# Kernel optimization log

Hardware: AMD Instinct MI355X
Metric: run time of the kernel (lower is better)

## Reference

```python
import jax, jax.numpy as jnp
import numpy as np

EPS = 1e-10


def _entropy(feat):
    # feat: [B,S,D] -> [B,S]
    fa = jnp.abs(feat)
    fn = fa / (fa.sum(axis=-1, keepdims=True) + EPS)
    return -jnp.sum(fn * jnp.log(fn + EPS), axis=-1)


def setup_inputs() -> dict:
    key = jax.random.key(0)
    ks = jax.random.split(key, 16)
    B, S, H, C = 16, 1024, 512, 7
    inp = {
        'text': jax.random.normal(ks[0], (B, S, H), dtype=jnp.float32),
        'audio': jax.random.normal(ks[1], (B, S, H), dtype=jnp.float32),
        'visual': jax.random.normal(ks[2], (B, S, H), dtype=jnp.float32),
        'speaker_graph': jax.random.uniform(ks[3], (B, S, S), dtype=jnp.float32),
        'temporal_graph': jax.random.uniform(ks[4], (B, S, S), dtype=jnp.float32),
        'qmask': jax.random.randint(ks[5], (B, S), 0, 9, dtype=jnp.int64),
        # entropy gate linear: in = 3H+1, out = H  (stored as [in,out])
        'gate_W': jax.random.normal(ks[6], (3 * H + 1, H), dtype=jnp.float32) * 0.02,
        'gate_b': jnp.zeros((H,), dtype=jnp.float32),
        # spectral conv layers
        'W0': jax.random.normal(ks[7], (3 * H, H), dtype=jnp.float32) * 0.02,
        'b0': jnp.zeros((H,), dtype=jnp.float32),
        'W1': jax.random.normal(ks[8], (H, H), dtype=jnp.float32) * 0.02,
        'b1': jnp.zeros((H,), dtype=jnp.float32),
        'W2': jax.random.normal(ks[9], (H, H), dtype=jnp.float32) * 0.02,
        'b2': jnp.zeros((H,), dtype=jnp.float32),
        # classifier
        'Wc': jax.random.normal(ks[10], (H, C), dtype=jnp.float32) * 0.02,
        'bc': jnp.zeros((C,), dtype=jnp.float32),
    }
    return inp


def reference(text, audio, visual, speaker_graph, temporal_graph, qmask,
              gate_W, gate_b, W0, b0, W1, b1, W2, b2, Wc, bc):
    feats = {'text': text, 'audio': audio, 'visual': visual}
    names = list(feats.keys())

    # per-node entropy on speaker graph path (entropy_t computed but unused, as in source)
    ent_s = {m: _entropy(f) for m, f in feats.items()}

    # entropy-weighted gating per modality
    fused = {}
    for m in names:
        feat = feats[m]
        ref = jnp.mean(jnp.stack([feats[o] for o in names if o != m], axis=-1), axis=-1)
        gi = jnp.concatenate([feat, feat, ref, ent_s[m][..., None]], axis=-1)  # [B,S,3H+1]
        gate = jax.nn.sigmoid(gi @ gate_W + gate_b)
        fused[m] = gate * feat

    # spectral GNN: symmetric-normalized fused adjacency with self loops
    B, S = text.shape[0], text.shape[1]
    fused_adj = 0.5 * speaker_graph + 0.5 * temporal_graph
    fused_adj = fused_adj + jnp.eye(S, dtype=fused_adj.dtype)[None]
    D = fused_adj.sum(axis=-1)                                   # [B,S]
    dsi = jax.lax.rsqrt(D + EPS)                                  # (D+eps)^-0.5
    norm_adj = dsi[:, :, None] * fused_adj * dsi[:, None, :]      # [B,S,S]

    h = jnp.concatenate([fused['text'], fused['audio'], fused['visual']], axis=-1)  # [B,S,3H]
    for W, b in ((W0, b0), (W1, b1), (W2, b2)):
        h = jax.nn.relu(jnp.einsum('bij,bjd->bid', norm_adj, h @ W) + b)

    return h @ Wc + bc
```

## Files before the change

kernel.cpp:

```cpp
#include <hip/hip_runtime.h>
#include <hip/hip_bf16.h>
#include <hip/hip_fp16.h>

typedef _Float16 f16;
typedef __attribute__((ext_vector_type(8))) _Float16 f16x8;
typedef __attribute__((ext_vector_type(4))) _Float16 f16x4;
typedef __attribute__((ext_vector_type(4))) float f32x4;
typedef __attribute__((address_space(1))) const unsigned int gu32;
typedef __attribute__((address_space(3))) unsigned int lu32;

#define BQ 16
#define SQ 1024
#define HQ 512
#define MQ (BQ*SQ)
#define PLANE ((size_t)MQ*512)

#define OFF_WG1T 0ul
#define OFF_WG2T 524288ul
#define OFF_W0T  1048576ul
#define OFF_W1T  2621440ul
#define OFF_W2T  3145728ul
#define OFF_WENT 3670016ul
#define OFF_ENTS 3672064ul
#define OFF_DSI  3868672ul
#define OFF_XF16 3934208ul
#define OFF_ANORM OFF_XF16
#define OFF_HN   (OFF_XF16 + 33554432ul)
#define OFF_T    71043072ul
#define OFF_YT   OFF_T
#define OFF_HCAT 104597504ul

__device__ __forceinline__ void gl16(f16* lds, const f16* g) {
    __builtin_amdgcn_global_load_lds(
        (gu32*)(const __attribute__((address_space(1))) f16*)g,
        (lu32*)(__attribute__((address_space(3))) f16*)lds, 16, 0, 0);
}

__global__ __launch_bounds__(256) void k_prep(
    const float* __restrict__ gW, const float* __restrict__ W0,
    const float* __restrict__ W1, const float* __restrict__ W2,
    f16* __restrict__ Wg1t, f16* __restrict__ Wg2t, f16* __restrict__ W0t,
    f16* __restrict__ W1t, f16* __restrict__ W2t, float* __restrict__ went)
{
    int i = blockIdx.x * 256 + threadIdx.x;
    if (i < 1536*512) {
        int n = i & 511, k = i >> 9;
        W0t[(size_t)n*1536 + k] = (f16)W0[(size_t)k*512 + n];
    }
    if (i < 512*512) {
        int n = i >> 9, k = i & 511;
        float wa = gW[(size_t)k*512 + n];
        float wb = gW[(size_t)(512 + k)*512 + n];
        float wr = gW[(size_t)(1024 + k)*512 + n];
        Wg1t[(size_t)n*512 + k] = (f16)(wa + wb - 0.5f*wr);
        Wg2t[(size_t)n*512 + k] = (f16)(0.5f*wr);
        W1t[(size_t)n*512 + k]  = (f16)W1[(size_t)k*512 + n];
        W2t[(size_t)n*512 + k]  = (f16)W2[(size_t)k*512 + n];
    }
    if (i < 512) went[i] = gW[(size_t)1536*512 + i];
}

__global__ __launch_bounds__(256) void k_ent(
    const float* __restrict__ t, const float* __restrict__ a, const float* __restrict__ v,
    f16* __restrict__ xf, float* __restrict__ ents)
{
    int wave = threadIdx.x >> 6, lane = threadIdx.x & 63;
    int row = blockIdx.x * 4 + wave;
    const float* ptrs[3] = {t, a, v};
    float sum8[8];
#pragma unroll
    for (int j = 0; j < 8; j++) sum8[j] = 0.f;
#pragma unroll
    for (int m = 0; m < 3; m++) {
        const float4* p = (const float4*)(ptrs[m] + (size_t)row*512);
        float4 x0 = p[lane*2], x1 = p[lane*2 + 1];
        float xs[8] = {x0.x,x0.y,x0.z,x0.w,x1.x,x1.y,x1.z,x1.w};
        float s = 0.f;
#pragma unroll
        for (int j = 0; j < 8; j++) s += fabsf(xs[j]);
#pragma unroll
        for (int off = 32; off; off >>= 1) s += __shfl_xor(s, off);
        float inv = 1.f / (s + 1e-10f);
        float e = 0.f;
#pragma unroll
        for (int j = 0; j < 8; j++) { float fn = fabsf(xs[j])*inv; e += fn*__logf(fn + 1e-10f); }
#pragma unroll
        for (int off = 32; off; off >>= 1) e += __shfl_xor(e, off);
        if (lane == 0) ents[m*MQ + row] = -e;
        f16x8 o;
#pragma unroll
        for (int j = 0; j < 8; j++) o[j] = (f16)xs[j];
        *(f16x8*)(xf + ((size_t)m*MQ + row)*512 + lane*8) = o;
#pragma unroll
        for (int j = 0; j < 8; j++) sum8[j] += xs[j];
    }
    f16x8 o;
#pragma unroll
    for (int j = 0; j < 8; j++) o[j] = (f16)sum8[j];
    *(f16x8*)(xf + ((size_t)3*MQ + row)*512 + lane*8) = o;
}

__global__ __launch_bounds__(256) void k_dsi(
    const float* __restrict__ sp, const float* __restrict__ tg, float* __restrict__ dsi)
{
    int wave = threadIdx.x >> 6, lane = threadIdx.x & 63;
    int row = blockIdx.x * 4 + wave;
    const float4* p1 = (const float4*)(sp + (size_t)row*1024);
    const float4* p2 = (const float4*)(tg + (size_t)row*1024);
    float s = 0.f;
#pragma unroll
    for (int c = 0; c < 4; c++) {
        float4 x = p1[c*64 + lane], y = p2[c*64 + lane];
        s += x.x + x.y + x.z + x.w + y.x + y.y + y.z + y.w;
    }
#pragma unroll
    for (int off = 32; off; off >>= 1) s += __shfl_xor(s, off);
    if (lane == 0) dsi[row] = 1.f / sqrtf(0.5f*s + 1.f + 1e-10f);
}

__global__ __launch_bounds__(256) void k_anorm(
    const float* __restrict__ sp, const float* __restrict__ tg,
    const float* __restrict__ dsi, f16* __restrict__ an)
{
    size_t t = (size_t)blockIdx.x*256 + threadIdx.x;
    int j4 = (int)(t & 255) * 4;
    int i  = (int)(t >> 8) & 1023;
    int b  = (int)(t >> 18);
    size_t base = ((size_t)b << 20) + (size_t)i*1024 + j4;
    float4 x = *(const float4*)(sp + base);
    float4 y = *(const float4*)(tg + base);
    float4 dj = *(const float4*)(dsi + b*1024 + j4);
    float di = dsi[b*1024 + i];
    float v0 = 0.5f*(x.x + y.x) + (i == j4+0 ? 1.f : 0.f);
    float v1 = 0.5f*(x.y + y.y) + (i == j4+1 ? 1.f : 0.f);
    float v2 = 0.5f*(x.z + y.z) + (i == j4+2 ? 1.f : 0.f);
    float v3 = 0.5f*(x.w + y.w) + (i == j4+3 ? 1.f : 0.f);
    f16x4 o;
    o[0] = (f16)(di*v0*dj.x); o[1] = (f16)(di*v1*dj.y);
    o[2] = (f16)(di*v2*dj.z); o[3] = (f16)(di*v3*dj.w);
    *(f16x4*)(an + base) = o;
}

template<int MODE>
__global__ __launch_bounds__(256) void k_gemm(
    const f16* __restrict__ A, const f16* __restrict__ Bt, int K,
    const f16* __restrict__ Tbuf, const float* __restrict__ entS,
    const float* __restrict__ went, const float* __restrict__ gb,
    const f16* __restrict__ featf, f16* __restrict__ hOut, int hColOff,
    const float* __restrict__ bias)
{
    __shared__ f16 As[128*64];
    __shared__ f16 Bs[128*64];
    int tid = threadIdx.x;
    int lane = tid & 63, wave = tid >> 6;
    int wr = wave >> 1, wc = wave & 1;
    int m0 = blockIdx.x * 128, n0 = blockIdx.y * 128;
    int z = blockIdx.z;
    if constexpr (MODE == 3) {
        A  += (size_t)z * (1024*1024);
        Bt += (size_t)z * (512*1024);
    }
    int lrow = lane >> 3;
    int swz  = (lane & 7) ^ lrow;
    const f16* pA = A  + (size_t)(m0 + wave*32 + lrow)*K + swz*8;
    const f16* pB = Bt + (size_t)(n0 + wave*32 + lrow)*K + swz*8;
    f16* lA = As + (wave*4)*512;
    f16* lB = Bs + (wave*4)*512;

    f32x4 acc[4][4];
#pragma unroll
    for (int mi = 0; mi < 4; mi++)
#pragma unroll
        for (int ni = 0; ni < 4; ni++) acc[mi][ni] = (f32x4){0.f,0.f,0.f,0.f};
    int g = lane >> 4, r = lane & 15;

    for (int kt = 0; kt < K; kt += 64) {
        __syncthreads();
#pragma unroll
        for (int j = 0; j < 4; j++) {
            gl16(lA + j*512, pA + (size_t)(j*8)*K + kt);
            gl16(lB + j*512, pB + (size_t)(j*8)*K + kt);
        }
        __syncthreads();
#pragma unroll
        for (int kk = 0; kk < 2; kk++) {
            f16x8 af[4], bf[4];
#pragma unroll
            for (int mi = 0; mi < 4; mi++) {
                int row = wr*64 + mi*16 + r;
                int ch = (kk*4 + g) ^ (row & 7);
                af[mi] = *(const f16x8*)&As[row*64 + ch*8];
            }
#pragma unroll
            for (int ni = 0; ni < 4; ni++) {
                int row = wc*64 + ni*16 + r;
                int ch = (kk*4 + g) ^ (row & 7);
                bf[ni] = *(const f16x8*)&Bs[row*64 + ch*8];
            }
#pragma unroll
            for (int mi = 0; mi < 4; mi++)
#pragma unroll
                for (int ni = 0; ni < 4; ni++)
                    acc[mi][ni] = __builtin_amdgcn_mfma_f32_16x16x32_f16(af[mi], bf[ni], acc[mi][ni], 0, 0, 0);
        }
    }
#pragma unroll
    for (int mi = 0; mi < 4; mi++) {
        int row0 = m0 + wr*64 + mi*16 + g*4;
#pragma unroll
        for (int ni = 0; ni < 4; ni++) {
            int col = n0 + wc*64 + ni*16 + r;
            f32x4 v = acc[mi][ni];
            if constexpr (MODE == 0) {
#pragma unroll
                for (int j = 0; j < 4; j++)
                    hOut[(size_t)(row0 + j)*512 + col] = (f16)v[j];
            } else if constexpr (MODE == 1) {
                float wcol = went[col], gbc = gb[col];
#pragma unroll
                for (int j = 0; j < 4; j++) {
                    int row = row0 + j;
                    float val = v[j] + (float)Tbuf[(size_t)row*512 + col] + entS[row]*wcol + gbc;
                    float gate = 1.f / (1.f + __expf(-val));
                    float o = gate * (float)featf[(size_t)row*512 + col];
                    hOut[(size_t)row*1536 + hColOff + col] = (f16)o;
                }
            } else if constexpr (MODE == 2) {
                int bb = row0 >> 10, ml = row0 & 1023;
                f16x4 h4;
#pragma unroll
                for (int j = 0; j < 4; j++) h4[j] = (f16)v[j];
                *(f16x4*)(hOut + (((size_t)(bb*512 + col)) << 10) + ml) = h4;
            } else {
                float bcol = bias[col];
#pragma unroll
                for (int j = 0; j < 4; j++) {
                    float o = v[j] + bcol;
                    o = o > 0.f ? o : 0.f;
                    hOut[(size_t)(z*1024 + row0 + j)*512 + col] = (f16)o;
                }
            }
        }
    }
}

__global__ __launch_bounds__(256) void k_cls(
    const f16* __restrict__ h, const float* __restrict__ Wc,
    const float* __restrict__ bc, float* __restrict__ out)
{
    int wave = threadIdx.x >> 6, lane = threadIdx.x & 63;
    int row = blockIdx.x * 4 + wave;
    f16x8 hv = *(const f16x8*)(h + (size_t)row*512 + lane*8);
    float acc[7];
#pragma unroll
    for (int c = 0; c < 7; c++) acc[c] = 0.f;
#pragma unroll
    for (int j = 0; j < 8; j++) {
        float x = (float)hv[j];
        const float* wrow = Wc + (size_t)(lane*8 + j)*7;
#pragma unroll
        for (int c = 0; c < 7; c++) acc[c] += x * wrow[c];
    }
#pragma unroll
    for (int off = 32; off; off >>= 1)
#pragma unroll
        for (int c = 0; c < 7; c++) acc[c] += __shfl_xor(acc[c], off);
    if (lane == 0) {
#pragma unroll
        for (int c = 0; c < 7; c++) out[(size_t)row*7 + c] = acc[c] + bc[c];
    }
}

extern "C" void kernel_launch(void* const* d_in, const int* in_sizes, int n_in,
                              void* d_out, int out_size, void* d_ws, size_t ws_size,
                              hipStream_t stream) {
    (void)in_sizes; (void)n_in; (void)out_size; (void)ws_size;
    const float* text   = (const float*)d_in[0];
    const float* audio  = (const float*)d_in[1];
    const float* visual = (const float*)d_in[2];
    const float* spg    = (const float*)d_in[3];
    const float* tmg    = (const float*)d_in[4];
    const float* gW     = (const float*)d_in[6];
    const float* gb     = (const float*)d_in[7];
    const float* W0     = (const float*)d_in[8];
    const float* b0     = (const float*)d_in[9];
    const float* W1     = (const float*)d_in[10];
    const float* b1     = (const float*)d_in[11];
    const float* W2     = (const float*)d_in[12];
    const float* b2     = (const float*)d_in[13];
    const float* Wc     = (const float*)d_in[14];
    const float* bc     = (const float*)d_in[15];

    char* ws = (char*)d_ws;
    f16*   Wg1t = (f16*)(ws + OFF_WG1T);
    f16*   Wg2t = (f16*)(ws + OFF_WG2T);
    f16*   W0t  = (f16*)(ws + OFF_W0T);
    f16*   W1t  = (f16*)(ws + OFF_W1T);
    f16*   W2t  = (f16*)(ws + OFF_W2T);
    float* went = (float*)(ws + OFF_WENT);
    float* ents = (float*)(ws + OFF_ENTS);
    float* dsi  = (float*)(ws + OFF_DSI);
    f16*   xf   = (f16*)(ws + OFF_XF16);
    f16*   an   = (f16*)(ws + OFF_ANORM);
    f16*   hn   = (f16*)(ws + OFF_HN);
    f16*   Tbuf = (f16*)(ws + OFF_T);
    f16*   yt   = (f16*)(ws + OFF_YT);
    f16*   hcat = (f16*)(ws + OFF_HCAT);
    float* outp = (float*)d_out;

    dim3 blk(256);
    k_prep<<<3072, blk, 0, stream>>>(gW, W0, W1, W2, Wg1t, Wg2t, W0t, W1t, W2t, went);
    k_ent<<<4096, blk, 0, stream>>>(text, audio, visual, xf, ents);
    k_dsi<<<4096, blk, 0, stream>>>(spg, tmg, dsi);

    k_gemm<0><<<dim3(128,4), blk, 0, stream>>>(xf + 3*PLANE, Wg2t, 512,
        nullptr, nullptr, nullptr, nullptr, nullptr, Tbuf, 0, nullptr);
    k_gemm<1><<<dim3(128,4), blk, 0, stream>>>(xf + 0*PLANE, Wg1t, 512,
        Tbuf, ents + 0*MQ, went, gb, xf + 0*PLANE, hcat, 0,    nullptr);
    k_gemm<1><<<dim3(128,4), blk, 0, stream>>>(xf + 1*PLANE, Wg1t, 512,
        Tbuf, ents + 1*MQ, went, gb, xf + 1*PLANE, hcat, 512,  nullptr);
    k_gemm<1><<<dim3(128,4), blk, 0, stream>>>(xf + 2*PLANE, Wg1t, 512,
        Tbuf, ents + 2*MQ, went, gb, xf + 2*PLANE, hcat, 1024, nullptr);

    k_anorm<<<16384, blk, 0, stream>>>(spg, tmg, dsi, an);

    k_gemm<2><<<dim3(128,4), blk, 0, stream>>>(hcat, W0t, 1536,
        nullptr, nullptr, nullptr, nullptr, nullptr, yt, 0, nullptr);
    k_gemm<3><<<dim3(8,4,16), blk, 0, stream>>>(an, yt, 1024,
        nullptr, nullptr, nullptr, nullptr, nullptr, hn, 0, b0);
    k_gemm<2><<<dim3(128,4), blk, 0, stream>>>(hn, W1t, 512,
        nullptr, nullptr, nullptr, nullptr, nullptr, yt, 0, nullptr);
    k_gemm<3><<<dim3(8,4,16), blk, 0, stream>>>(an, yt, 1024,
        nullptr, nullptr, nullptr, nullptr, nullptr, hn, 0, b1);
    k_gemm<2><<<dim3(128,4), blk, 0, stream>>>(hn, W2t, 512,
        nullptr, nullptr, nullptr, nullptr, nullptr, yt, 0, nullptr);
    k_gemm<3><<<dim3(8,4,16), blk, 0, stream>>>(an, yt, 1024,
        nullptr, nullptr, nullptr, nullptr, nullptr, hn, 0, b2);

    k_cls<<<4096, blk, 0, stream>>>(hn, Wc, bc, outp);
}
```

Baseline: 551.8 us.

## Double-buffer GEMM shared-memory tiles and restructure entropy reduction

The GEMM kernel now uses two LDS buffers per operand. The global-to-LDS load of the next K tile is issued before the MFMA work on the current tile, with one barrier per iteration instead of two. This is meant to hide global load latency behind compute, at the cost of doubling LDS use (64KB per block), which may lower occupancy. The entropy kernel is also rewritten to compute the sum and the sum of a*log(a) in a single pass, then derive entropy algebraically. This lets the reductions for all three modalities be interleaved and removes the serial dependency between the two shuffle reductions.

```diff
diff --git a/kernel.cpp b/kernel.cpp
--- a/kernel.cpp
+++ b/kernel.cpp
@@ -67,32 +67,52 @@
     int wave = threadIdx.x >> 6, lane = threadIdx.x & 63;
     int row = blockIdx.x * 4 + wave;
     const float* ptrs[3] = {t, a, v};
-    float sum8[8];
-#pragma unroll
-    for (int j = 0; j < 8; j++) sum8[j] = 0.f;
+    float4 x[3][2];
 #pragma unroll
     for (int m = 0; m < 3; m++) {
         const float4* p = (const float4*)(ptrs[m] + (size_t)row*512);
-        float4 x0 = p[lane*2], x1 = p[lane*2 + 1];
-        float xs[8] = {x0.x,x0.y,x0.z,x0.w,x1.x,x1.y,x1.z,x1.w};
-        float s = 0.f;
-#pragma unroll
-        for (int j = 0; j < 8; j++) s += fabsf(xs[j]);
-#pragma unroll
-        for (int off = 32; off; off >>= 1) s += __shfl_xor(s, off);
-        float inv = 1.f / (s + 1e-10f);
-        float e = 0.f;
-#pragma unroll
-        for (int j = 0; j < 8; j++) { float fn = fabsf(xs[j])*inv; e += fn*__logf(fn + 1e-10f); }
-#pragma unroll
-        for (int off = 32; off; off >>= 1) e += __shfl_xor(e, off);
-        if (lane == 0) ents[m*MQ + row] = -e;
+        x[m][0] = p[lane*2];
+        x[m][1] = p[lane*2 + 1];
+    }
+    float s[3], tt[3];
+#pragma unroll
+    for (int m = 0; m < 3; m++) {
+        float xs[8] = {x[m][0].x,x[m][0].y,x[m][0].z,x[m][0].w,
+                       x[m][1].x,x[m][1].y,x[m][1].z,x[m][1].w};
+        s[m] = 0.f; tt[m] = 0.f;
+#pragma unroll
+        for (int j = 0; j < 8; j++) {
+            float ab = fabsf(xs[j]);
+            s[m]  += ab;
+            tt[m] += ab * __logf(ab + 1e-12f);
+        }
+    }
+#pragma unroll
+    for (int off = 32; off; off >>= 1) {
+#pragma unroll
+        for (int m = 0; m < 3; m++) {
+            s[m]  += __shfl_xor(s[m],  off);
+            tt[m] += __shfl_xor(tt[m], off);
+        }
+    }
+    if (lane == 0) {
+#pragma unroll
+        for (int m = 0; m < 3; m++) {
+            float sp = s[m] + 1e-10f;
+            ents[m*MQ + row] = __logf(sp) * (s[m]/sp) - tt[m]/sp;
+        }
+    }
+    float sum8[8];
+#pragma unroll
+    for (int j = 0; j < 8; j++) sum8[j] = 0.f;
+#pragma unroll
+    for (int m = 0; m < 3; m++) {
+        float xs[8] = {x[m][0].x,x[m][0].y,x[m][0].z,x[m][0].w,
+                       x[m][1].x,x[m][1].y,x[m][1].z,x[m][1].w};
         f16x8 o;
 #pragma unroll
-        for (int j = 0; j < 8; j++) o[j] = (f16)xs[j];
+        for (int j = 0; j < 8; j++) { o[j] = (f16)xs[j]; sum8[j] += xs[j]; }
         *(f16x8*)(xf + ((size_t)m*MQ + row)*512 + lane*8) = o;
-#pragma unroll
-        for (int j = 0; j < 8; j++) sum8[j] += xs[j];
     }
     f16x8 o;
 #pragma unroll
@@ -149,8 +169,8 @@
     const f16* __restrict__ featf, f16* __restrict__ hOut, int hColOff,
     const float* __restrict__ bias)
 {
-    __shared__ f16 As[128*64];
-    __shared__ f16 Bs[128*64];
+    __shared__ f16 As[2][128*64];
+    __shared__ f16 Bs[2][128*64];
     int tid = threadIdx.x;
     int lane = tid & 63, wave = tid >> 6;
     int wr = wave >> 1, wc = wave & 1;
@@ -164,8 +184,6 @@
     int swz  = (lane & 7) ^ lrow;
     const f16* pA = A  + (size_t)(m0 + wave*32 + lrow)*K + swz*8;
     const f16* pB = Bt + (size_t)(n0 + wave*32 + lrow)*K + swz*8;
-    f16* lA = As + (wave*4)*512;
-    f16* lB = Bs + (wave*4)*512;
 
     f32x4 acc[4][4];
 #pragma unroll
@@ -174,14 +192,24 @@
         for (int ni = 0; ni < 4; ni++) acc[mi][ni] = (f32x4){0.f,0.f,0.f,0.f};
     int g = lane >> 4, r = lane & 15;
 
-    for (int kt = 0; kt < K; kt += 64) {
-        __syncthreads();
-#pragma unroll
-        for (int j = 0; j < 4; j++) {
-            gl16(lA + j*512, pA + (size_t)(j*8)*K + kt);
-            gl16(lB + j*512, pB + (size_t)(j*8)*K + kt);
-        }
-        __syncthreads();
+    int NT = K >> 6;
+#pragma unroll
+    for (int j = 0; j < 4; j++) {
+        gl16(&As[0][(wave*4 + j)*512], pA + (size_t)(j*8)*K);
+        gl16(&Bs[0][(wave*4 + j)*512], pB + (size_t)(j*8)*K);
+    }
+    __syncthreads();
+
+    for (int t = 0; t < NT; ++t) {
+        int cur = t & 1;
+        if (t + 1 < NT) {
+            int nb = cur ^ 1, kt = (t + 1) << 6;
+#pragma unroll
+            for (int j = 0; j < 4; j++) {
+                gl16(&As[nb][(wave*4 + j)*512], pA + (size_t)(j*8)*K + kt);
+                gl16(&Bs[nb][(wave*4 + j)*512], pB + (size_t)(j*8)*K + kt);
+            }
+        }
 #pragma unroll
         for (int kk = 0; kk < 2; kk++) {
             f16x8 af[4], bf[4];
@@ -189,13 +217,13 @@
             for (int mi = 0; mi < 4; mi++) {
                 int row = wr*64 + mi*16 + r;
                 int ch = (kk*4 + g) ^ (row & 7);
-                af[mi] = *(const f16x8*)&As[row*64 + ch*8];
+                af[mi] = *(const f16x8*)&As[cur][row*64 + ch*8];
             }
 #pragma unroll
             for (int ni = 0; ni < 4; ni++) {
                 int row = wc*64 + ni*16 + r;
                 int ch = (kk*4 + g) ^ (row & 7);
-                bf[ni] = *(const f16x8*)&Bs[row*64 + ch*8];
+                bf[ni] = *(const f16x8*)&Bs[cur][row*64 + ch*8];
             }
 #pragma unroll
             for (int mi = 0; mi < 4; mi++)
@@ -203,6 +231,7 @@
                 for (int ni = 0; ni < 4; ni++)
                     acc[mi][ni] = __builtin_amdgcn_mfma_f32_16x16x32_f16(af[mi], bf[ni], acc[mi][ni], 0, 0, 0);
         }
+        __syncthreads();
     }
 #pragma unroll
     for (int mi = 0; mi < 4; mi++) {
```

Result: no change. 552.4 us (+0.1%).
